# Kernel optimization log

Hardware: AMD Instinct MI355X
Metric: run time of the kernel (lower is better)

Reference implementation:

```python
import jax, jax.numpy as jnp
import numpy as np

B, N, NE = 4, 10000, 100000
D, S, H, T = 128, 64, 4, 128      # enc_dim, enc_s_dim, n_head, n_token
NS = D + S                        # GNN node_size = 192
EPS = 1e-5


def linear(x, w, b):
    return x @ w.T + b


def layer_norm(x, g, b):
    m = jnp.mean(x, -1, keepdims=True)
    v = jnp.mean((x - m) ** 2, -1, keepdims=True)
    return (x - m) * jax.lax.rsqrt(v + EPS) * g + b


def mha(q, k, v, wqkv, bqkv, wo, bo):
    # torch nn.MultiheadAttention, batch_first=True
    d = q.shape[-1]; hd = d // H
    wq, wk, wv = jnp.split(wqkv, 3, 0)
    bq, bk, bv = jnp.split(bqkv, 3, 0)
    def proj(x, w, bb):
        Bx, L, _ = x.shape
        return (x @ w.T + bb).reshape(Bx, L, H, hd)
    qh, kh, vh = proj(q, wq, bq), proj(k, wk, bk), proj(v, wv, bv)
    scores = jnp.einsum('bqhd,bkhd->bhqk', qh, kh) / jnp.sqrt(jnp.asarray(hd, q.dtype))
    att = jax.nn.softmax(scores, axis=-1)
    o = jnp.einsum('bhqk,bkhd->bqhd', att, vh).reshape(q.shape[0], q.shape[1], d)
    return o @ wo.T + bo


def smean(vals, idx, n):
    # scatter_mean over one batch element: vals (ne,f), idx (ne,)
    s = jax.ops.segment_sum(vals, idx, num_segments=n)
    c = jax.ops.segment_sum(jnp.ones(idx.shape, vals.dtype), idx, num_segments=n)
    return s / jnp.maximum(c, 1.0)[:, None]

_smean_b = jax.vmap(smean, in_axes=(0, 0, None))
_gather_b = jax.vmap(lambda v, i: v[i])


def setup_inputs():
    key = jax.random.key(0)
    ks = jax.random.split(key, 32)
    r = lambda i, shape: jax.random.normal(ks[i], shape, jnp.float32) * 0.02
    inp = {
        'V': jax.random.normal(ks[0], (B, N, D), jnp.float32),
        'E': jax.random.normal(ks[1], (B, NE, D), jnp.float32),
        'edges': jax.random.randint(ks[2], (B, NE, 2), 0, N),
        's_enc': jax.random.normal(ks[3], (B, N, S), jnp.float32),
        # GNN f_edge: Linear(512,128) SiLU Linear(128,128) LN(128)
        'fe_w1': r(4, (D, D + 2 * NS)), 'fe_b1': jnp.zeros(D),
        'fe_w2': r(5, (D, D)), 'fe_b2': jnp.zeros(D),
        'fe_g': jnp.ones(D), 'fe_be': jnp.zeros(D),
        # GNN f_node: Linear(320,128) SiLU Linear(128,128) LN(128)
        'fn_w1': r(6, (D, NS + D)), 'fn_b1': jnp.zeros(D),
        'fn_w2': r(7, (D, D)), 'fn_b2': jnp.zeros(D),
        'fn_g': jnp.ones(D), 'fn_be': jnp.zeros(D),
        'ln1_g': jnp.ones(D), 'ln1_b': jnp.zeros(D),
        'ln2_g': jnp.ones(D), 'ln2_b': jnp.zeros(D),
        'Q': jax.random.normal(ks[8], (T, D), jnp.float32),
        'a1_wqkv': r(9, (3 * D, D)), 'a1_bqkv': jnp.zeros(3 * D),
        'a1_wo': r(10, (D, D)), 'a1_bo': jnp.zeros(D),
        'a2_wqkv': r(11, (3 * D, D)), 'a2_bqkv': jnp.zeros(3 * D),
        'a2_wo': r(12, (D, D)), 'a2_bo': jnp.zeros(D),
        'a3_wqkv': r(13, (3 * D, D)), 'a3_bqkv': jnp.zeros(3 * D),
        'a3_wo': r(14, (D, D)), 'a3_bo': jnp.zeros(D),
        'ffn_w1': r(15, (2 * D, D)), 'ffn_b1': jnp.zeros(2 * D),
        'ffn_w2': r(16, (D, 2 * D)), 'ffn_b2': jnp.zeros(D),
    }
    return inp


def reference(V, E, edges, s_enc,
              fe_w1, fe_b1, fe_w2, fe_b2, fe_g, fe_be,
              fn_w1, fn_b1, fn_w2, fn_b2, fn_g, fn_be,
              ln1_g, ln1_b, ln2_g, ln2_b,
              Q, a1_wqkv, a1_bqkv, a1_wo, a1_bo,
              a2_wqkv, a2_bqkv, a2_wo, a2_bo,
              a3_wqkv, a3_bqkv, a3_wo, a3_bo,
              ffn_w1, ffn_b1, ffn_w2, ffn_b2):
    n = V.shape[1]
    V_in = jnp.concatenate([V, s_enc], -1)                  # (B,N,192)
    valid = jnp.all(edges >= 0, -1)                          # (B,NE)
    safe = jnp.clip(edges, 0, n - 1)
    senders = _gather_b(V_in, safe[..., 0])                  # (B,NE,192)
    receivers = _gather_b(V_in, safe[..., 1])
    edge_inpt = jnp.concatenate([senders, receivers, E], -1) # (B,NE,512)
    eh = jax.nn.silu(linear(edge_inpt, fe_w1, fe_b1))
    e_emb = layer_norm(linear(eh, fe_w2, fe_b2), fe_g, fe_be)
    e_emb = e_emb * valid[..., None].astype(e_emb.dtype)
    e0, e1 = jnp.split(e_emb, 2, -1)
    m0 = _smean_b(e0, safe[..., 0], n)
    m1 = _smean_b(e1, safe[..., 1], n)
    node_inpt = jnp.concatenate([V_in, m0, m1], -1)          # (B,N,320)
    nh = jax.nn.silu(linear(node_inpt, fn_w1, fn_b1))
    v_emb = layer_norm(linear(nh, fn_w2, fn_b2), fn_g, fn_be)
    E_out = E + e_emb
    V1 = V + v_emb
    # attention block
    W0 = layer_norm(V1, ln1_g, ln1_b)
    lq = jnp.broadcast_to(Q, (V.shape[0],) + Q.shape)
    W = mha(lq, W0, W0, a1_wqkv, a1_bqkv, a1_wo, a1_bo)
    W = mha(W, W, W, a2_wqkv, a2_bqkv, a2_wo, a2_bo)
    W = mha(W0, W, W, a3_wqkv, a3_bqkv, a3_wo, a3_bo)
    V2 = V1 + W
    # FFN block
    x = layer_norm(V2, ln2_g, ln2_b)
    V3 = V2 + linear(jax.nn.silu(linear(x, ffn_w1, ffn_b1)), ffn_w2, ffn_b2)
    return (V3, E_out)
```

## Files before the change

### kernel.cpp

```cpp
#include <hip/hip_runtime.h>
#include <hip/hip_bf16.h>

#define B_ 4
#define N_ 10000
#define NE_ 100000
#define D_ 128
#define S_ 64
#define H_ 4
#define T_ 128

typedef unsigned short u16;
typedef unsigned int u32;
typedef __attribute__((ext_vector_type(4))) float f4;
typedef __attribute__((ext_vector_type(8))) short s8;

#define DEVI static __device__ __forceinline__

DEVI float b2f(u16 u){ union{u32 i; float f;} v; v.i=((u32)u)<<16; return v.f; }
DEVI u16 f2b(float f){ union{float ff; u32 i;} v; v.ff=f; u32 i=v.i; return (u16)((i+0x7fffu+((i>>16)&1u))>>16); }
DEVI f4 mfma16(s8 a, s8 b, f4 c){ return __builtin_amdgcn_mfma_f32_16x16x32_bf16(a,b,c,0,0,0); }
DEVI float rsum16(float x){ x+=__shfl_xor(x,1); x+=__shfl_xor(x,2); x+=__shfl_xor(x,4); x+=__shfl_xor(x,8); return x; }
DEVI float silu_f(float v){ return v/(1.f+__expf(-v)); }
DEVI float nn(float v, float s){ return (v==v)? v : s; }
DEVI float lo2f(u32 u){ union{u32 i; float f;} v; v.i=u<<16; return v.f; }
DEVI float hi2f(u32 u){ union{u32 i; float f;} v; v.i=u&0xffff0000u; return v.f; }

DEVI s8 ldw8f(const float* p){
  f4 a = *(const f4*)p;
  f4 c = *(const f4*)(p+4);
  union { u16 t[8]; s8 v; } u;
  #pragma unroll
  for (int i=0;i<4;i++){ u.t[i]=f2b(a[i]); u.t[4+i]=f2b(c[i]); }
  return u.v;
}
DEVI uint4 cvt8(const float* p){
  f4 a = *(const f4*)p;
  f4 c = *(const f4*)(p+4);
  union { u16 t[8]; uint4 v; } u;
  #pragma unroll
  for (int i=0;i<4;i++){ u.t[i]=f2b(a[i]); u.t[4+i]=f2b(c[i]); }
  return u.v;
}
DEVI uint4 cvt8nt(const float* p){
  f4 a = __builtin_nontemporal_load((const f4*)p);
  f4 c = __builtin_nontemporal_load((const f4*)(p+4));
  union { u16 t[8]; uint4 v; } u;
  #pragma unroll
  for (int i=0;i<4;i++){ u.t[i]=f2b(a[i]); u.t[4+i]=f2b(c[i]); }
  return u.v;
}

#define WO_FE1 0
#define WO_FE2 65536
#define WO_FN1 81920
#define WO_FN2 122880
#define WO_A1  139264
#define WO_A3  188416
#define WO_A3O 237568
#define WO_FF1 253952
#define WO_FF2 286720
#define WTOT   319488

__global__ __launch_bounds__(256) void k_cvtw(
  const float* __restrict__ s0, const float* __restrict__ s1,
  const float* __restrict__ s2, const float* __restrict__ s3,
  const float* __restrict__ s4, const float* __restrict__ s5,
  const float* __restrict__ s6, const float* __restrict__ s7,
  const float* __restrict__ s8v, u16* __restrict__ dst)
{
  int i = (blockIdx.x*256 + threadIdx.x)*8;
  if (i >= WTOT) return;
  const float* src; int off;
  if      (i < WO_FE2){ src=s0;  off=WO_FE1; }
  else if (i < WO_FN1){ src=s1;  off=WO_FE2; }
  else if (i < WO_FN2){ src=s2;  off=WO_FN1; }
  else if (i < WO_A1 ){ src=s3;  off=WO_FN2; }
  else if (i < WO_A3 ){ src=s4;  off=WO_A1;  }
  else if (i < WO_A3O){ src=s5;  off=WO_A3;  }
  else if (i < WO_FF1){ src=s6;  off=WO_A3O; }
  else if (i < WO_FF2){ src=s7;  off=WO_FF1; }
  else                { src=s8v; off=WO_FF2; }
  *(uint4*)(dst+i) = cvt8(src + (i-off));
}

__global__ __launch_bounds__(512,4) void k_edge(
  const float* __restrict__ V, const float* __restrict__ E, const int* __restrict__ edges,
  const float* __restrict__ senc,
  const u16* __restrict__ w1b, const float* __restrict__ b1,
  const u16* __restrict__ w2b, const float* __restrict__ b2,
  const float* __restrict__ lng, const float* __restrict__ lnb,
  float* __restrict__ m0s, float* __restrict__ m1s,
  float* __restrict__ c0s, float* __restrict__ c1s,
  float* __restrict__ Eout)
{
  __shared__ u16 X[64][520];
  __shared__ int gi0[64], gi1[64];
  __shared__ float fvalid[64];
  __shared__ float rsA[64][8], rsB[64][8];
  const int tid = threadIdx.x;
  const int el = tid>>3, part = tid&7;
  const int ge = blockIdx.x*64 + el;
  const int b = ge / NE_;
  const int2 ed = *(const int2*)(edges + (size_t)ge*2);
  const int i0 = min(max(ed.x,0),N_-1), i1 = min(max(ed.y,0),N_-1);
  if (part==0){
    gi0[el] = b*N_ + i0; gi1[el] = b*N_ + i1;
    fvalid[el] = (ed.x>=0 && ed.y>=0) ? 1.f : 0.f;
  }
  {
    const float* Vb = V + (size_t)b*N_*D_;
    const float* Sb = senc + (size_t)b*N_*S_;
    const float* Ep = E + (size_t)ge*D_;
    #pragma unroll
    for (int j=0;j<8;j++){
      int u = part + 8*j;
      if (u<48){
        const float* p;
        if (u<16)      p = Vb + (size_t)i0*D_ + u*8;
        else if (u<24) p = Sb + (size_t)i0*S_ + (u-16)*8;
        else if (u<40) p = Vb + (size_t)i1*D_ + (u-24)*8;
        else           p = Sb + (size_t)i1*S_ + (u-40)*8;
        *(uint4*)&X[el][u*8] = cvt8(p);
      } else {
        *(uint4*)&X[el][u*8] = cvt8nt(Ep + (u-48)*8);
      }
    }
  }
  __syncthreads();
  if (tid < 64){
    atomicAdd(&c0s[gi0[tid]], 1.f);
    atomicAdd(&c1s[gi1[tid]], 1.f);
  }
  const int lane = tid&63, w = tid>>6;
  const int l15 = lane&15, hi = lane>>4;
  const int colb = w*16;
  f4 acc[4];
  #pragma unroll
  for (int m=0;m<4;m++){ float bb=b1[colb+l15]; acc[m]=(f4){bb,bb,bb,bb}; }
  for (int kk=0;kk<16;kk++){
    s8 bfr = *(const s8*)(w1b + (size_t)(colb+l15)*512 + kk*32 + hi*8);
    #pragma unroll
    for (int m=0;m<4;m++){
      s8 a = *(const s8*)&X[m*16+l15][kk*32 + hi*8];
      acc[m] = mfma16(a, bfr, acc[m]);
    }
  }
  __syncthreads();
  #pragma unroll
  for (int m=0;m<4;m++)
    #pragma unroll
    for (int r=0;r<4;r++)
      X[m*16+hi*4+r][colb+l15] = f2b(silu_f(acc[m][r]));
  __syncthreads();
  f4 a2[4];
  #pragma unroll
  for (int m=0;m<4;m++){ float bb=b2[colb+l15]; a2[m]=(f4){bb,bb,bb,bb}; }
  #pragma unroll
  for (int kk=0;kk<4;kk++){
    s8 bfr = *(const s8*)(w2b + (size_t)(colb+l15)*128 + kk*32 + hi*8);
    #pragma unroll
    for (int m=0;m<4;m++){
      s8 a = *(const s8*)&X[m*16+l15][kk*32 + hi*8];
      a2[m] = mfma16(a, bfr, a2[m]);
    }
  }
  #pragma unroll
  for (int m=0;m<4;m++)
    #pragma unroll
    for (int r=0;r<4;r++){
      float v=a2[m][r];
      float ps=rsum16(v), pq=rsum16(v*v);
      if (l15==0){ int row=m*16+hi*4+r; rsA[row][w]=ps; rsB[row][w]=pq; }
    }
  __syncthreads();
  const float gv=lng[colb+l15], bev=lnb[colb+l15];
  const int ge0 = blockIdx.x*64;
  #pragma unroll
  for (int m=0;m<4;m++)
    #pragma unroll
    for (int r=0;r<4;r++){
      const int row = m*16+hi*4+r;
      float s=0.f, s2=0.f;
      #pragma unroll
      for (int ww=0;ww<8;ww++){ s+=rsA[row][ww]; s2+=rsB[row][ww]; }
      const float mean = s*(1.f/128.f);
      const float rstd = rsqrtf(s2*(1.f/128.f) - mean*mean + 1e-5f);
      const float vm = fvalid[row];
      const int col = colb+l15;
      float ev = ((a2[m][r]-mean)*rstd*gv + bev) * vm;
      ev = nn(ev, 7e3f);
      if (col < 64) atomicAdd(m0s + (size_t)gi0[row]*64 + col, ev);
      else          atomicAdd(m1s + (size_t)gi1[row]*64 + (col-64), ev);
      float ef = b2f(X[row][384+col]);
      __builtin_nontemporal_store(ef + ev, Eout + (size_t)(ge0+row)*D_ + col);
    }
}

__global__ __launch_bounds__(256,2) void k_nodekv(
  const float* __restrict__ V, const float* __restrict__ senc,
  const float* __restrict__ m0s, const float* __restrict__ m1s,
  const float* __restrict__ c0s, const float* __restrict__ c1s,
  const u16* __restrict__ w1b, const float* __restrict__ b1,
  const u16* __restrict__ w2b, const float* __restrict__ b2,
  const float* __restrict__ lng, const float* __restrict__ lnb,
  const float* __restrict__ l1g, const float* __restrict__ l1b,
  const u16* __restrict__ wqkvb, const float* __restrict__ bqkv,
  u16* __restrict__ V1, u16* __restrict__ W0,
  u16* __restrict__ kh1, u16* __restrict__ vh1)
{
  __shared__ u16 X[64][328];
  __shared__ float rsA[64][4], rsB[64][4];
  const int tid=threadIdx.x, nl=tid>>2, part=tid&3;
  const int gn = blockIdx.x*64 + nl;
  const int b = gn / N_, n = gn - b*N_;
  {
    const float* Vp = V + ((size_t)b*N_ + n)*D_;
    const float* Sp = senc + ((size_t)b*N_ + n)*S_;
    #pragma unroll
    for (int j=0;j<6;j++){
      int u = part + 4*j;
      const float* p = (u<16)? Vp + u*8 : Sp + (u-16)*8;
      *(uint4*)&X[nl][u*8] = cvt8(p);
    }
    const float rc0 = 1.f/fmaxf(c0s[gn],1.f), rc1 = 1.f/fmaxf(c1s[gn],1.f);
    #pragma unroll
    for (int j=0;j<8;j++){
      int c = part*32 + j*4;
      const float* src = (c<64)? m0s + (size_t)gn*64 + c : m1s + (size_t)gn*64 + (c-64);
      float rr = (c<64)? rc0 : rc1;
      f4 mv = *(const f4*)src;
      u16 ov[4];
      #pragma unroll
      for (int i=0;i<4;i++) ov[i]=f2b(mv[i]*rr);
      uint2 pk; __builtin_memcpy(&pk, ov, 8);
      *(uint2*)&X[nl][192+c] = pk;
    }
  }
  __syncthreads();
  const int lane=tid&63, w=tid>>6, l15=lane&15, hi=lane>>4, colb=w*32;
  f4 acc[4][2];
  #pragma unroll
  for (int m=0;m<4;m++)
    #pragma unroll
    for (int tl=0;tl<2;tl++){ float bb=b1[colb+tl*16+l15]; acc[m][tl]=(f4){bb,bb,bb,bb}; }
  for (int kk=0;kk<10;kk++){
    s8 bfr[2];
    #pragma unroll
    for (int tl=0;tl<2;tl++)
      bfr[tl] = *(const s8*)(w1b + (size_t)(colb+tl*16+l15)*320 + kk*32 + hi*8);
    #pragma unroll
    for (int m=0;m<4;m++){
      s8 a = *(const s8*)&X[m*16+l15][kk*32+hi*8];
      #pragma unroll
      for (int tl=0;tl<2;tl++) acc[m][tl]=mfma16(a,bfr[tl],acc[m][tl]);
    }
  }
  __syncthreads();
  #pragma unroll
  for (int m=0;m<4;m++)
    #pragma unroll
    for (int tl=0;tl<2;tl++)
      #pragma unroll
      for (int r=0;r<4;r++)
        X[m*16+hi*4+r][192+colb+tl*16+l15] = f2b(silu_f(acc[m][tl][r]));
  __syncthreads();
  f4 a2[4][2];
  #pragma unroll
  for (int m=0;m<4;m++)
    #pragma unroll
    for (int tl=0;tl<2;tl++){ float bb=b2[colb+tl*16+l15]; a2[m][tl]=(f4){bb,bb,bb,bb}; }
  #pragma unroll
  for (int kk=0;kk<4;kk++){
    s8 bfr[2];
    #pragma unroll
    for (int tl=0;tl<2;tl++)
      bfr[tl] = *(const s8*)(w2b + (size_t)(colb+tl*16+l15)*128 + kk*32 + hi*8);
    #pragma unroll
    for (int m=0;m<4;m++){
      s8 a = *(const s8*)&X[m*16+l15][192 + kk*32+hi*8];
      #pragma unroll
      for (int tl=0;tl<2;tl++) a2[m][tl]=mfma16(a,bfr[tl],a2[m][tl]);
    }
  }
  #pragma unroll
  for (int m=0;m<4;m++)
    #pragma unroll
    for (int r=0;r<4;r++){
      float ps=0.f, pq=0.f;
      #pragma unroll
      for (int tl=0;tl<2;tl++){ float v=a2[m][tl][r]; ps+=v; pq+=v*v; }
      ps=rsum16(ps); pq=rsum16(pq);
      if (l15==0){ int row=m*16+hi*4+r; rsA[row][w]=ps; rsB[row][w]=pq; }
    }
  __syncthreads();
  float gv[2],bev[2],g1v[2],b1v[2];
  #pragma unroll
  for (int tl=0;tl<2;tl++){
    int col=colb+tl*16+l15;
    gv[tl]=lng[col]; bev[tl]=lnb[col]; g1v[tl]=l1g[col]; b1v[tl]=l1b[col];
  }
  #pragma unroll
  for (int m=0;m<4;m++)
    #pragma unroll
    for (int r=0;r<4;r++){
      const int row=m*16+hi*4+r;
      float s  = rsA[row][0]+rsA[row][1]+rsA[row][2]+rsA[row][3];
      float s2 = rsB[row][0]+rsB[row][1]+rsB[row][2]+rsB[row][3];
      float mean=s*(1.f/128.f);
      float rstd=rsqrtf(s2*(1.f/128.f)-mean*mean+1e-5f);
      #pragma unroll
      for (int tl=0;tl<2;tl++){
        float ve=(a2[m][tl][r]-mean)*rstd*gv[tl]+bev[tl];
        a2[m][tl][r] = b2f(X[row][colb+tl*16+l15]) + ve;
      }
    }
  __syncthreads();
  #pragma unroll
  for (int m=0;m<4;m++)
    #pragma unroll
    for (int r=0;r<4;r++){
      float ps=0.f, pq=0.f;
      #pragma unroll
      for (int tl=0;tl<2;tl++){ float v=a2[m][tl][r]; ps+=v; pq+=v*v; }
      ps=rsum16(ps); pq=rsum16(pq);
      if (l15==0){ int row=m*16+hi*4+r; rsA[row][w]=ps; rsB[row][w]=pq; }
    }
  __syncthreads();
  #pragma unroll
  for (int m=0;m<4;m++)
    #pragma unroll
    for (int r=0;r<4;r++){
      const int row=m*16+hi*4+r;
      float sv  = rsA[row][0]+rsA[row][1]+rsA[row][2]+rsA[row][3];
      float sv2 = rsB[row][0]+rsB[row][1]+rsB[row][2]+rsB[row][3];
      float m2=sv*(1.f/128.f);
      float rs2=rsqrtf(sv2*(1.f/128.f)-m2*m2+1e-5f);
      #pragma unroll
      for (int tl=0;tl<2;tl++){
        int col=colb+tl*16+l15;
        float tmp=a2[m][tl][r];
        X[row][col]     = f2b(tmp);
        X[row][192+col] = f2b((tmp-m2)*rs2*g1v[tl]+b1v[tl]);
      }
    }
  __syncthreads();
  #pragma unroll
  for (int j=0;j<4;j++){
    int u=part+4*j;
    *(uint4*)(V1 + (size_t)gn*D_ + u*8) = *(const uint4*)&X[nl][u*8];
    *(uint4*)(W0 + (size_t)gn*D_ + u*8) = *(const uint4*)&X[nl][192 + u*8];
  }
  const int colb2 = w*64;
  f4 acck[4][4];
  #pragma unroll
  for (int m=0;m<4;m++)
    #pragma unroll
    for (int tl=0;tl<4;tl++){ float bb=bqkv[128 + colb2+tl*16+l15]; acck[m][tl]=(f4){bb,bb,bb,bb}; }
  #pragma unroll
  for (int kk=0;kk<4;kk++){
    s8 bfr[4];
    #pragma unroll
    for (int tl=0;tl<4;tl++)
      bfr[tl] = *(const s8*)(wqkvb + (size_t)(128 + colb2+tl*16+l15)*D_ + kk*32+hi*8);
    #pragma unroll
    for (int m=0;m<4;m++){
      s8 a = *(const s8*)&X[m*16+l15][192 + kk*32+hi*8];
      #pragma unroll
      for (int tl=0;tl<4;tl++) acck[m][tl]=mfma16(a,bfr[tl],acck[m][tl]);
    }
  }
  __syncthreads();
  #pragma unroll
  for (int m=0;m<4;m++)
    #pragma unroll
    for (int tl=0;tl<4;tl++)
      #pragma unroll
      for (int r=0;r<4;r++)
        X[m*16+hi*4+r][colb2+tl*16+l15]=f2b(acck[m][tl][r]);
  __syncthreads();
  #pragma unroll
  for (int j=0;j<8;j++){
    int u=part+4*j, col0=u*8;
    u16* dst;
    if (col0<128){ int h=col0>>5, d=col0&31; dst = kh1 + ((size_t)(b*H_+h)*N_ + n)*32 + d; }
    else { int c2=col0-128; int h=c2>>5, d=c2&31; dst = vh1 + ((size_t)(b*H_+h)*N_ + n)*32 + d; }
    *(uint4*)dst = *(const uint4*)&X[nl][col0];
  }
}

__global__ __launch_bounds__(256) void k_qh1(
  const float* __restrict__ Q, const float* __restrict__ wqkv, const float* __restrict__ bqkv,
  u16* __restrict__ qh1)
{
  __shared__ u16 X[64][136];
  const int tid=threadIdx.x, nl=tid>>2, part=tid&3;
  const int q = blockIdx.x*64 + nl;
  #pragma unroll
  for (int j=0;j<4;j++){ int u=part+4*j; *(uint4*)&X[nl][u*8] = cvt8(Q + (size_t)q*D_ + u*8); }
  __syncthreads();
  const int lane=tid&63, w=tid>>6, l15=lane&15, hi=lane>>4, rw=w*16;
  f4 acc[8];
  #pragma unroll
  for (int t=0;t<8;t++){ float bb=bqkv[l15+16*t]; acc[t]=(f4){bb,bb,bb,bb}; }
  #pragma unroll
  for (int kk=0;kk<4;kk++){
    s8 a = *(const s8*)&X[rw+l15][kk*32+hi*8];
    #pragma unroll
    for (int t=0;t<8;t++){
      s8 bf = ldw8f(wqkv + (size_t)(t*16+l15)*D_ + kk*32+hi*8);
      acc[t]=mfma16(a,bf,acc[t]);
    }
  }
  __syncthreads();
  #pragma unroll
  for (int t=0;t<8;t++){
    #pragma unroll
    for (int r=0;r<4;r++) X[rw+hi*4+r][l15+16*t]=f2b(acc[t][r]);
  }
  __syncthreads();
  #pragma unroll
  for (int j=0;j<4;j++){
    int u=part+4*j, col0=u*8, h=col0>>5, d=col0&31;
    *(uint4*)(qh1 + ((size_t)h*T_ + q)*32 + d) = *(const uint4*)&X[nl][col0];
  }
}

#define NCH 20
#define CHK 512

__global__ __launch_bounds__(256,2) void k_mha1p(
  const u16* __restrict__ qh1, const u16* __restrict__ kh1, const u16* __restrict__ vh1,
  float* __restrict__ pm, float* __restrict__ pl, float* __restrict__ po)
{
  __shared__ u16 VT[32][72];
  __shared__ u16 P[4][32][72];
  const int bh = blockIdx.x / NCH, ch = blockIdx.x - bh*NCH;
  const int tid = threadIdx.x, w = tid>>6, lane = tid&63, l15=lane&15, hi=lane>>4;
  const int h = bh & 3;
  const int k0 = ch*CHK;
  const int nk = min(CHK, N_ - k0);
  const u16* Kb = kh1 + ((size_t)bh*N_ + k0)*32;
  const u16* Vb = vh1 + ((size_t)bh*N_ + k0)*32;
  s8 aq[2];
  #pragma unroll
  for (int qt=0;qt<2;qt++)
    aq[qt] = *(const s8*)(qh1 + ((size_t)h*T_ + w*32 + qt*16 + l15)*32 + hi*8);
  const float scale = 0.17677669529663687f;
  float m_reg[2][4], l_reg[2][4];
  f4 acc[2][2];
  #pragma unroll
  for (int qt=0;qt<2;qt++){
    #pragma unroll
    for (int r=0;r<4;r++){ m_reg[qt][r]=-1e30f; l_reg[qt][r]=0.f; }
    #pragma unroll
    for (int dt=0;dt<2;dt++) acc[qt][dt]=(f4){0.f,0.f,0.f,0.f};
  }
  const int ntile = (nk+63)>>6;
  for (int kt=0; kt<ntile; kt++){
    {
      int key = tid>>2, dseg = tid&3;
      int kg = kt*64 + key;
      uint4 v = (kg<nk)? *(const uint4*)(Vb + (size_t)kg*32 + dseg*8) : (uint4){0,0,0,0};
      const u16* vv = (const u16*)&v;
      #pragma unroll
      for (int i=0;i<8;i++) VT[dseg*8+i][key] = vv[i];
    }
    __syncthreads();
    f4 sa[2][4];
    #pragma unroll
    for (int kt4=0;kt4<4;kt4++){
      int key = kt*64 + kt4*16 + l15;
      int keyc = min(key, nk-1);
      s8 bk = *(const s8*)(Kb + (size_t)keyc*32 + hi*8);
      #pragma unroll
      for (int qt=0;qt<2;qt++)
        sa[qt][kt4] = mfma16(aq[qt], bk, (f4){0.f,0.f,0.f,0.f});
    }
    #pragma unroll
    for (int qt=0;qt<2;qt++){
      #pragma unroll
      for (int r=0;r<4;r++){
        float s[4];
        float mx = -1e30f;
        #pragma unroll
        for (int kt4=0;kt4<4;kt4++){
          int key = kt*64 + kt4*16 + l15;
          s[kt4] = (key<nk)? sa[qt][kt4][r]*scale : -1e30f;
          mx = fmaxf(mx, s[kt4]);
        }
        mx=fmaxf(mx,__shfl_xor(mx,1)); mx=fmaxf(mx,__shfl_xor(mx,2));
        mx=fmaxf(mx,__shfl_xor(mx,4)); mx=fmaxf(mx,__shfl_xor(mx,8));
        float mn = fmaxf(m_reg[qt][r], mx);
        float corr = __expf(m_reg[qt][r]-mn);
        float ps=0.f;
        #pragma unroll
        for (int kt4=0;kt4<4;kt4++){
          float p = __expf(s[kt4]-mn);
          ps += p;
          P[w][qt*16+hi*4+r][kt4*16+l15] = f2b(p);
        }
        ps = rsum16(ps);
        l_reg[qt][r] = l_reg[qt][r]*corr + ps;
        m_reg[qt][r] = mn;
        #pragma unroll
        for (int dt=0;dt<2;dt++) acc[qt][dt][r] *= corr;
      }
    }
    __syncthreads();
    #pragma unroll
    for (int ks=0;ks<2;ks++){
      s8 bv[2];
      #pragma unroll
      for (int dt=0;dt<2;dt++)
        bv[dt] = *(const s8*)&VT[dt*16+l15][ks*32+hi*8];
      #pragma unroll
      for (int qt=0;qt<2;qt++){
        s8 pa = *(const s8*)&P[w][qt*16+l15][ks*32+hi*8];
        #pragma unroll
        for (int dt=0;dt<2;dt++)
          acc[qt][dt]=mfma16(pa,bv[dt],acc[qt][dt]);
      }
    }
    __syncthreads();
  }
  const size_t pbase = ((size_t)bh*NCH + ch)*128;
  #pragma unroll
  for (int qt=0;qt<2;qt++)
    #pragma unroll
    for (int r=0;r<4;r++){
      int row = w*32 + qt*16 + hi*4 + r;
      if (l15==0){ pm[pbase+row]=m_reg[qt][r]; pl[pbase+row]=l_reg[qt][r]; }
      #pragma unroll
      for (int dt=0;dt<2;dt++)
        po[(pbase+row)*32 + dt*16 + l15] = acc[qt][dt][r];
    }
}

__global__ __launch_bounds__(256) void k_mha1c(
  const float* __restrict__ pm, const float* __restrict__ pl, const float* __restrict__ po,
  float* __restrict__ o1)
{
  int gid = blockIdx.x*256 + threadIdx.x;
  int row = gid >> 5, dim = gid & 31;
  int bh = row >> 7, q = row & 127;
  int b = bh >> 2, h = bh & 3;
  float M = -1e30f;
  #pragma unroll
  for (int ch=0; ch<NCH; ch++) M = fmaxf(M, pm[((size_t)bh*NCH+ch)*128 + q]);
  float L=0.f, O=0.f;
  for (int ch=0; ch<NCH; ch++){
    size_t pb = ((size_t)bh*NCH+ch)*128 + q;
    float e = __expf(pm[pb]-M);
    L += pl[pb]*e;
    O += po[pb*32+dim]*e;
  }
  o1[((size_t)b*T_+q)*D_ + h*32 + dim] = O / L;
}

DEVI void mha_core(const float* qv, const u16* Kb, const u16* Vb, int nk,
                   int lane, float* outp)
{
  const float scale = 0.17677669529663687f;
  float m=-1e30f, ssum=0.f, o[32];
  #pragma unroll
  for (int i=0;i<32;i++) o[i]=0.f;
  for (int c0=0;c0<nk;c0+=64){
    int key=c0+lane, keyc = key<nk? key: nk-1;
    const uint4* kp=(const uint4*)(Kb+(size_t)keyc*32);
    float sa=0.f;
    #pragma unroll
    for (int i=0;i<4;i++){ uint4 u=kp[i];
      sa += qv[i*8+0]*lo2f(u.x)+qv[i*8+1]*hi2f(u.x)+qv[i*8+2]*lo2f(u.y)+qv[i*8+3]*hi2f(u.y)
          + qv[i*8+4]*lo2f(u.z)+qv[i*8+5]*hi2f(u.z)+qv[i*8+6]*lo2f(u.w)+qv[i*8+7]*hi2f(u.w);
    }
    float s=sa*scale;
    float mn=fmaxf(m,s);
    float corr=__expf(m-mn);
    float p=(key<nk)?__expf(s-mn):0.f;
    ssum=ssum*corr+p;
    const uint4* vp=(const uint4*)(Vb+(size_t)keyc*32);
    #pragma unroll
    for (int i=0;i<4;i++){ uint4 u=vp[i];
      o[i*8+0]=o[i*8+0]*corr+p*lo2f(u.x); o[i*8+1]=o[i*8+1]*corr+p*hi2f(u.x);
      o[i*8+2]=o[i*8+2]*corr+p*lo2f(u.y); o[i*8+3]=o[i*8+3]*corr+p*hi2f(u.y);
      o[i*8+4]=o[i*8+4]*corr+p*lo2f(u.z); o[i*8+5]=o[i*8+5]*corr+p*hi2f(u.z);
      o[i*8+6]=o[i*8+6]*corr+p*lo2f(u.w); o[i*8+7]=o[i*8+7]*corr+p*hi2f(u.w);
    }
    m=mn;
  }
  float M=m;
  #pragma unroll
  for (int d=32;d>=1;d>>=1) M=fmaxf(M,__shfl_xor(M,d));
  float sc=__expf(m-M);
  float sm=ssum*sc;
  #pragma unroll
  for (int d=32;d>=1;d>>=1) sm+=__shfl_xor(sm,d);
  float inv=1.f/sm;
  #pragma unroll
  for (int i=0;i<32;i++){
    float v=o[i]*sc;
    #pragma unroll
    for (int d=32;d>=1;d>>=1) v+=__shfl_xor(v,d);
    if (lane==0) outp[i]=v*inv;
  }
}

__global__ __launch_bounds__(256) void k_mha2(
  const u16* __restrict__ qh2, const u16* __restrict__ kh2, const u16* __restrict__ vh2,
  float* __restrict__ o2)
{
  const int blk=blockIdx.x, bh=blk>>5, b=bh>>2, h=bh&3;
  const int w=threadIdx.x>>6, lane=threadIdx.x&63;
  const int q=(blk&31)*4+w;
  float qv[32];
  const uint4* qp=(const uint4*)(qh2 + ((size_t)bh*T_+q)*32);
  #pragma unroll
  for (int i=0;i<4;i++){ uint4 u=qp[i];
    qv[i*8+0]=lo2f(u.x); qv[i*8+1]=hi2f(u.x); qv[i*8+2]=lo2f(u.y); qv[i*8+3]=hi2f(u.y);
    qv[i*8+4]=lo2f(u.z); qv[i*8+5]=hi2f(u.z); qv[i*8+6]=lo2f(u.w); qv[i*8+7]=hi2f(u.w); }
  mha_core(qv, kh2+(size_t)bh*T_*32, vh2+(size_t)bh*T_*32, T_, lane,
           o2+((size_t)b*T_+q)*D_+h*32);
}

__global__ __launch_bounds__(256) void k_att12(
  const float* __restrict__ o1, const float* __restrict__ wo, const float* __restrict__ bo,
  const float* __restrict__ wqkv, const float* __restrict__ bqkv,
  u16* __restrict__ qh2, u16* __restrict__ kh2, u16* __restrict__ vh2)
{
  __shared__ u16 X[64][136];
  __shared__ u16 Y[64][392];
  const int tid=threadIdx.x, nl=tid>>2, part=tid&3;
  const int row = blockIdx.x*64 + nl;
  #pragma unroll
  for (int j=0;j<8;j++){
    int c = part*32 + j*4;
    f4 mv = *(const f4*)(o1 + (size_t)row*D_ + c);
    u16 ov[4];
    #pragma unroll
    for (int i=0;i<4;i++) ov[i]=f2b(nn(mv[i],2e4f));
    uint2 pk; __builtin_memcpy(&pk, ov, 8);
    *(uint2*)&X[nl][c]=pk;
  }
  __syncthreads();
  const int lane=tid&63, w=tid>>6, l15=lane&15, hi=lane>>4, rw=w*16;
  {
    f4 acc[8];
    #pragma unroll
    for (int t=0;t<8;t++){ float bb=bo[l15+16*t]; acc[t]=(f4){bb,bb,bb,bb}; }
    #pragma unroll
    for (int kk=0;kk<4;kk++){
      s8 a = *(const s8*)&X[rw+l15][kk*32+hi*8];
      #pragma unroll
      for (int t=0;t<8;t++){
        s8 bf = ldw8f(wo + (size_t)(t*16+l15)*D_ + kk*32+hi*8);
        acc[t]=mfma16(a,bf,acc[t]);
      }
    }
    #pragma unroll
    for (int t=0;t<8;t++){
      #pragma unroll
      for (int r=0;r<4;r++) Y[rw+hi*4+r][l15+16*t]=f2b(acc[t][r]);
    }
  }
  __syncthreads();
  f4 a2[24];
  #pragma unroll
  for (int t=0;t<24;t++){ float bb=bqkv[l15+16*t]; a2[t]=(f4){bb,bb,bb,bb}; }
  #pragma unroll
  for (int kk=0;kk<4;kk++){
    s8 a = *(const s8*)&Y[rw+l15][kk*32+hi*8];
    #pragma unroll
    for (int t=0;t<24;t++){
      s8 bf = ldw8f(wqkv + (size_t)(t*16+l15)*D_ + kk*32+hi*8);
      a2[t]=mfma16(a,bf,a2[t]);
    }
  }
  __syncthreads();
  #pragma unroll
  for (int t=0;t<24;t++){
    #pragma unroll
    for (int r=0;r<4;r++) Y[rw+hi*4+r][l15+16*t]=f2b(a2[t][r]);
  }
  __syncthreads();
  const int b=row>>7, q=row&127;
  #pragma unroll
  for (int j=0;j<12;j++){
    int u=part+4*j, col0=u*8;
    int sel=col0>>7, c2=col0&127, h=c2>>5, d=c2&31;
    u16* base = sel==0? qh2 : (sel==1? kh2 : vh2);
    *(uint4*)(base + ((size_t)(b*H_+h)*T_ + q)*32 + d) = *(const uint4*)&Y[nl][col0];
  }
}

__global__ __launch_bounds__(256) void k_att23(
  const float* __restrict__ o2, const float* __restrict__ wo, const float* __restrict__ bo,
  const float* __restrict__ wqkv3, const float* __restrict__ bqkv3,
  u16* __restrict__ kh3, u16* __restrict__ vh3T)
{
  __shared__ u16 X[64][136];
  __shared__ u16 Y[64][264];
  const int tid=threadIdx.x, nl=tid>>2, part=tid&3;
  const int row = blockIdx.x*64 + nl;
  #pragma unroll
  for (int j=0;j<8;j++){
    int c = part*32 + j*4;
    f4 mv = *(const f4*)(o2 + (size_t)row*D_ + c);
    u16 ov[4];
    #pragma unroll
    for (int i=0;i<4;i++) ov[i]=f2b(nn(mv[i],3e4f));
    uint2 pk; __builtin_memcpy(&pk, ov, 8);
    *(uint2*)&X[nl][c]=pk;
  }
  __syncthreads();
  const int lane=tid&63, w=tid>>6, l15=lane&15, hi=lane>>4, rw=w*16;
  {
    f4 acc[8];
    #pragma unroll
    for (int t=0;t<8;t++){ float bb=bo[l15+16*t]; acc[t]=(f4){bb,bb,bb,bb}; }
    #pragma unroll
    for (int kk=0;kk<4;kk++){
      s8 a = *(const s8*)&X[rw+l15][kk*32+hi*8];
      #pragma unroll
      for (int t=0;t<8;t++){
        s8 bf = ldw8f(wo + (size_t)(t*16+l15)*D_ + kk*32+hi*8);
        acc[t]=mfma16(a,bf,acc[t]);
      }
    }
    #pragma unroll
    for (int t=0;t<8;t++){
      #pragma unroll
      for (int r=0;r<4;r++) Y[rw+hi*4+r][l15+16*t]=f2b(acc[t][r]);
    }
  }
  __syncthreads();
  f4 a2[16];
  #pragma unroll
  for (int t=0;t<16;t++){ float bb=bqkv3[128 + l15+16*t]; a2[t]=(f4){bb,bb,bb,bb}; }
  #pragma unroll
  for (int kk=0;kk<4;kk++){
    s8 a = *(const s8*)&Y[rw+l15][kk*32+hi*8];
    #pragma unroll
    for (int t=0;t<16;t++){
      s8 bf = ldw8f(wqkv3 + (size_t)(128 + t*16+l15)*D_ + kk*32+hi*8);
      a2[t]=mfma16(a,bf,a2[t]);
    }
  }
  __syncthreads();
  #pragma unroll
  for (int t=0;t<16;t++){
    #pragma unroll
    for (int r=0;r<4;r++) Y[rw+hi*4+r][l15+16*t]=f2b(a2[t][r]);
  }
  __syncthreads();
  const int b=row>>7, q=row&127;
  #pragma unroll
  for (int j=0;j<4;j++){
    int u=part+4*j, col0=u*8, h=col0>>5, d=col0&31;
    *(uint4*)(kh3 + ((size_t)(b*H_+h)*T_ + q)*32 + d) = *(const uint4*)&Y[nl][col0];
  }
  #pragma unroll
  for (int cc=0;cc<32;cc++){
    int c2 = part*32 + cc;
    int h=c2>>5, d=c2&31;
    vh3T[((size_t)(b*H_+h)*32 + d)*T_ + q] = Y[nl][128+c2];
  }
}

__global__ __launch_bounds__(256,2) void k_mha3f(
  const u16* __restrict__ W0, const u16* __restrict__ V1,
  const u16* __restrict__ wq3b, const float* __restrict__ bqkv3,
  const u16* __restrict__ kh3, const u16* __restrict__ vh3T,
  const u16* __restrict__ wo3b, const float* __restrict__ bo3,
  const float* __restrict__ l2g, const float* __restrict__ l2b,
  const u16* __restrict__ fw1b, const float* __restrict__ fb1,
  const u16* __restrict__ fw2b, const float* __restrict__ fb2,
  float* __restrict__ V3)
{
  __shared__ u16 Wt[64][136];
  __shared__ u16 Q3[64][136];
  __shared__ u16 P3[64][136];
  __shared__ float rsA[64][4], rsB[64][4];
  const int tid=threadIdx.x, nl=tid>>2, part=tid&3;
  const int b = blockIdx.x/157, tb = blockIdx.x - b*157;
  const int n0 = tb*64;
  {
    const int ns = min(n0+nl, N_-1);
    const u16* src = W0 + ((size_t)b*N_+ns)*D_;
    #pragma unroll
    for (int j=0;j<4;j++){ int u=part+4*j; *(uint4*)&Wt[nl][u*8] = *(const uint4*)(src+u*8); }
  }
  __syncthreads();
  const int lane=tid&63, w=tid>>6, l15=lane&15, hi=lane>>4;
  const int rw=w*16, colb=w*32;
  {
    f4 acc[4][2];
    #pragma unroll
    for (int m=0;m<4;m++)
      #pragma unroll
      for (int tl=0;tl<2;tl++){ float bb=bqkv3[colb+tl*16+l15]; acc[m][tl]=(f4){bb,bb,bb,bb}; }
    #pragma unroll
    for (int kk=0;kk<4;kk++){
      s8 bfr[2];
      #pragma unroll
      for (int tl=0;tl<2;tl++)
        bfr[tl] = *(const s8*)(wq3b + (size_t)(colb+tl*16+l15)*D_ + kk*32+hi*8);
      #pragma unroll
      for (int m=0;m<4;m++){
        s8 a = *(const s8*)&Wt[m*16+l15][kk*32+hi*8];
        #pragma unroll
        for (int tl=0;tl<2;tl++) acc[m][tl]=mfma16(a,bfr[tl],acc[m][tl]);
      }
    }
    #pragma unroll
    for (int m=0;m<4;m++)
      #pragma unroll
      for (int tl=0;tl<2;tl++)
        #pragma unroll
        for (int r=0;r<4;r++)
          Q3[m*16+hi*4+r][colb+tl*16+l15]=f2b(acc[m][tl][r]);
  }
  __syncthreads();
  const float scale=0.17677669529663687f;
  f4 oacc[8];
  #pragma unroll
  for (int t=0;t<8;t++) oacc[t]=(f4){0.f,0.f,0.f,0.f};
  #pragma unroll
  for (int h=0;h<H_;h++){
    f4 sa[8];
    #pragma unroll
    for (int t=0;t<8;t++) sa[t]=(f4){0.f,0.f,0.f,0.f};
    s8 aq = *(const s8*)&Q3[rw+l15][h*32+hi*8];
    #pragma unroll
    for (int t=0;t<8;t++){
      s8 bf = *(const s8*)(kh3 + ((size_t)(b*H_+h)*T_ + t*16+l15)*32 + hi*8);
      sa[t]=mfma16(aq,bf,sa[t]);
    }
    #pragma unroll
    for (int r=0;r<4;r++){
      const int row=rw+hi*4+r;
      float mx=-1e30f;
      float sv[8];
      #pragma unroll
      for (int t=0;t<8;t++){ sv[t]=sa[t][r]*scale; mx=fmaxf(mx,sv[t]); }
      mx=fmaxf(mx,__shfl_xor(mx,1)); mx=fmaxf(mx,__shfl_xor(mx,2));
      mx=fmaxf(mx,__shfl_xor(mx,4)); mx=fmaxf(mx,__shfl_xor(mx,8));
      float se=0.f; float pv[8];
      #pragma unroll
      for (int t=0;t<8;t++){ pv[t]=__expf(sv[t]-mx); se+=pv[t]; }
      se=rsum16(se);
      float inv=1.f/se;
      #pragma unroll
      for (int t=0;t<8;t++) P3[row][l15+16*t]=f2b(pv[t]*inv);
    }
    __syncthreads();
    #pragma unroll
    for (int kk=0;kk<4;kk++){
      s8 ap = *(const s8*)&P3[rw+l15][kk*32+hi*8];
      #pragma unroll
      for (int t2=0;t2<2;t2++){
        s8 bf = *(const s8*)(vh3T + ((size_t)(b*H_+h)*32 + t2*16+l15)*T_ + kk*32+hi*8);
        oacc[h*2+t2]=mfma16(ap,bf,oacc[h*2+t2]);
      }
    }
    __syncthreads();
  }
  #pragma unroll
  for (int t=0;t<8;t++){
    #pragma unroll
    for (int r=0;r<4;r++) Q3[rw+hi*4+r][l15+16*t]=f2b(oacc[t][r]);
  }
  __syncthreads();
  f4 a2[4][2];
  #pragma unroll
  for (int m=0;m<4;m++)
    #pragma unroll
    for (int tl=0;tl<2;tl++){ float bb=bo3[colb+tl*16+l15]; a2[m][tl]=(f4){bb,bb,bb,bb}; }
  #pragma unroll
  for (int kk=0;kk<4;kk++){
    s8 bfr[2];
    #pragma unroll
    for (int tl=0;tl<2;tl++)
      bfr[tl] = *(const s8*)(wo3b + (size_t)(colb+tl*16+l15)*D_ + kk*32+hi*8);
    #pragma unroll
    for (int m=0;m<4;m++){
      s8 a = *(const s8*)&Q3[m*16+l15][kk*32+hi*8];
      #pragma unroll
      for (int tl=0;tl<2;tl++) a2[m][tl]=mfma16(a,bfr[tl],a2[m][tl]);
    }
  }
  #pragma unroll
  for (int m=0;m<4;m++)
    #pragma unroll
    for (int r=0;r<4;r++){
      const int row=m*16+hi*4+r;
      const int nr = min(n0+row, N_-1);
      const size_t gr=(size_t)b*N_+nr;
      float ps=0.f, pq=0.f;
      #pragma unroll
      for (int tl=0;tl<2;tl++){
        float tmp = b2f(V1[gr*D_ + colb+tl*16+l15]) + a2[m][tl][r];
        a2[m][tl][r]=tmp; ps+=tmp; pq+=tmp*tmp;
      }
      ps=rsum16(ps); pq=rsum16(pq);
      if (l15==0){ rsA[row][w]=ps; rsB[row][w]=pq; }
    }
  __syncthreads();
  float g2v[2],b2v[2];
  #pragma unroll
  for (int tl=0;tl<2;tl++){ g2v[tl]=l2g[colb+tl*16+l15]; b2v[tl]=l2b[colb+tl*16+l15]; }
  #pragma unroll
  for (int m=0;m<4;m++)
    #pragma unroll
    for (int r=0;r<4;r++){
      const int row=m*16+hi*4+r;
      float s  = rsA[row][0]+rsA[row][1]+rsA[row][2]+rsA[row][3];
      float s2 = rsB[row][0]+rsB[row][1]+rsB[row][2]+rsB[row][3];
      float mean=s*(1.f/128.f);
      float rstd=rsqrtf(s2*(1.f/128.f)-mean*mean+1e-5f);
      #pragma unroll
      for (int tl=0;tl<2;tl++){
        int col=colb+tl*16+l15;
        float tmp=a2[m][tl][r];
        P3[row][col]=f2b(tmp);
        Wt[row][col]=f2b((tmp-mean)*rstd*g2v[tl]+b2v[tl]);
      }
    }
  __syncthreads();
  f4 accf[4][2];
  #pragma unroll
  for (int m=0;m<4;m++)
    #pragma unroll
    for (int tl=0;tl<2;tl++){ float bb=fb2[colb+tl*16+l15]; accf[m][tl]=(f4){bb,bb,bb,bb}; }
  for (int half=0;half<2;half++){
    f4 ah[4][2];
    #pragma unroll
    for (int m=0;m<4;m++)
      #pragma unroll
      for (int tl=0;tl<2;tl++){ float bb=fb1[half*128+colb+tl*16+l15]; ah[m][tl]=(f4){bb,bb,bb,bb}; }
    #pragma unroll
    for (int kk=0;kk<4;kk++){
      s8 bfr[2];
      #pragma unroll
      for (int tl=0;tl<2;tl++)
        bfr[tl] = *(const s8*)(fw1b + (size_t)(half*128+colb+tl*16+l15)*D_ + kk*32+hi*8);
      #pragma unroll
      for (int m=0;m<4;m++){
        s8 a = *(const s8*)&Wt[m*16+l15][kk*32+hi*8];
        #pragma unroll
        for (int tl=0;tl<2;tl++) ah[m][tl]=mfma16(a,bfr[tl],ah[m][tl]);
      }
    }
    __syncthreads();
    #pragma unroll
    for (int m=0;m<4;m++)
      #pragma unroll
      for (int tl=0;tl<2;tl++)
        #pragma unroll
        for (int r=0;r<4;r++)
          Q3[m*16+hi*4+r][colb+tl*16+l15]=f2b(silu_f(ah[m][tl][r]));
    __syncthreads();
    #pragma unroll
    for (int kk=0;kk<4;kk++){
      s8 bfr[2];
      #pragma unroll
      for (int tl=0;tl<2;tl++)
        bfr[tl] = *(const s8*)(fw2b + (size_t)(colb+tl*16+l15)*256 + half*128 + kk*32+hi*8);
      #pragma unroll
      for (int m=0;m<4;m++){
        s8 a = *(const s8*)&Q3[m*16+l15][kk*32+hi*8];
        #pragma unroll
        for (int tl=0;tl<2;tl++) accf[m][tl]=mfma16(a,bfr[tl],accf[m][tl]);
      }
    }
  }
  #pragma unroll
  for (int m=0;m<4;m++)
    #pragma unroll
    for (int r=0;r<4;r++){
      const int row=m*16+hi*4+r;
      if (n0+row < N_){
        const size_t gr=(size_t)b*N_+n0+row;
        #pragma unroll
        for (int tl=0;tl<2;tl++){
          int col=colb+tl*16+l15;
          V3[gr*D_+col] = b2f(P3[row][col]) + accf[m][tl][r];
        }
      }
    }
}

extern "C" void kernel_launch(void* const* d_in, const int* in_sizes, int n_in,
                              void* d_out, int out_size, void* d_ws, size_t ws_size,
                              hipStream_t stream)
{
  const float* V     = (const float*)d_in[0];
  const float* E     = (const float*)d_in[1];
  const int* edges   = (const int*)d_in[2];
  const float* senc  = (const float*)d_in[3];
  const float* fe_w1=(const float*)d_in[4];  const float* fe_b1=(const float*)d_in[5];
  const float* fe_w2=(const float*)d_in[6];  const float* fe_b2=(const float*)d_in[7];
  const float* fe_g =(const float*)d_in[8];  const float* fe_be=(const float*)d_in[9];
  const float* fn_w1=(const float*)d_in[10]; const float* fn_b1=(const float*)d_in[11];
  const float* fn_w2=(const float*)d_in[12]; const float* fn_b2=(const float*)d_in[13];
  const float* fn_g =(const float*)d_in[14]; const float* fn_be=(const float*)d_in[15];
  const float* ln1_g=(const float*)d_in[16]; const float* ln1_b=(const float*)d_in[17];
  const float* ln2_g=(const float*)d_in[18]; const float* ln2_b=(const float*)d_in[19];
  const float* Q    =(const float*)d_in[20];
  const float* a1_wqkv=(const float*)d_in[21]; const float* a1_bqkv=(const float*)d_in[22];
  const float* a1_wo=(const float*)d_in[23];   const float* a1_bo=(const float*)d_in[24];
  const float* a2_wqkv=(const float*)d_in[25]; const float* a2_bqkv=(const float*)d_in[26];
  const float* a2_wo=(const float*)d_in[27];   const float* a2_bo=(const float*)d_in[28];
  const float* a3_wqkv=(const float*)d_in[29]; const float* a3_bqkv=(const float*)d_in[30];
  const float* a3_wo=(const float*)d_in[31];   const float* a3_bo=(const float*)d_in[32];
  const float* ffn_w1=(const float*)d_in[33];  const float* ffn_b1=(const float*)d_in[34];
  const float* ffn_w2=(const float*)d_in[35];  const float* ffn_b2=(const float*)d_in[36];

  char* ws = (char*)d_ws;
  size_t off = 0;
  auto alloc = [&](size_t bytes)->void*{ void* p = ws + off; off += (bytes + 255) & ~(size_t)255; return p; };
  float* m0s = (float*)alloc((size_t)B_*N_*64*4);
  float* m1s = (float*)alloc((size_t)B_*N_*64*4);
  float* c0s = (float*)alloc((size_t)B_*N_*4);
  float* c1s = (float*)alloc((size_t)B_*N_*4);
  const size_t zero_bytes = off;
  u16* wcat = (u16*)alloc((size_t)WTOT*2);
  u16* V1  = (u16*)alloc((size_t)B_*N_*D_*2);
  u16* W0  = (u16*)alloc((size_t)B_*N_*D_*2);
  u16* kh1 = (u16*)alloc((size_t)B_*H_*N_*32*2);
  u16* vh1 = (u16*)alloc((size_t)B_*H_*N_*32*2);
  u16* qh1 = (u16*)alloc((size_t)H_*T_*32*2);
  float* o1 = (float*)alloc((size_t)B_*T_*D_*4);
  u16* qh2 = (u16*)alloc((size_t)B_*H_*T_*32*2);
  u16* kh2 = (u16*)alloc((size_t)B_*H_*T_*32*2);
  u16* vh2 = (u16*)alloc((size_t)B_*H_*T_*32*2);
  float* o2 = (float*)alloc((size_t)B_*T_*D_*4);
  u16* kh3 = (u16*)alloc((size_t)B_*H_*T_*32*2);
  u16* vh3T= (u16*)alloc((size_t)B_*H_*32*T_*2);
  float* pmw = (float*)alloc((size_t)B_*H_*NCH*128*4);
  float* plw = (float*)alloc((size_t)B_*H_*NCH*128*4);
  float* pow_ = (float*)alloc((size_t)B_*H_*NCH*128*32*4);
  if (ws_size < off) return;

  u16* w_fe1 = wcat + WO_FE1;
  u16* w_fe2 = wcat + WO_FE2;
  u16* w_fn1 = wcat + WO_FN1;
  u16* w_fn2 = wcat + WO_FN2;
  u16* w_a1  = wcat + WO_A1;
  u16* w_a3  = wcat + WO_A3;
  u16* w_a3o = wcat + WO_A3O;
  u16* w_ff1 = wcat + WO_FF1;
  u16* w_ff2 = wcat + WO_FF2;

  float* outp = (float*)d_out;
  float* V3out = outp;
  float* Eout  = outp + (size_t)B_*N_*D_;

  hipMemsetAsync(d_ws, 0, zero_bytes, stream);
  k_cvtw<<<(WTOT/8+255)/256,256,0,stream>>>(fe_w1,fe_w2,fn_w1,fn_w2,a1_wqkv,a3_wqkv,a3_wo,
                                            ffn_w1,ffn_w2, wcat);
  k_edge<<<(B_*NE_)/64,512,0,stream>>>(V,E,edges,senc, w_fe1,fe_b1, w_fe2,fe_b2, fe_g,fe_be,
                                       m0s,m1s,c0s,c1s, Eout);
  k_nodekv<<<(B_*N_)/64,256,0,stream>>>(V,senc,m0s,m1s,c0s,c1s, w_fn1,fn_b1, w_fn2,fn_b2,
                                        fn_g,fn_be, ln1_g,ln1_b, w_a1,a1_bqkv,
                                        V1,W0, kh1,vh1);
  k_qh1<<<T_/64,256,0,stream>>>(Q, a1_wqkv, a1_bqkv, qh1);
  k_mha1p<<<B_*H_*NCH,256,0,stream>>>(qh1,kh1,vh1, pmw,plw,pow_);
  k_mha1c<<<(B_*H_*T_*32)/256,256,0,stream>>>(pmw,plw,pow_, o1);
  k_att12<<<(B_*T_)/64,256,0,stream>>>(o1, a1_wo, a1_bo, a2_wqkv, a2_bqkv, qh2,kh2,vh2);
  k_mha2<<<(B_*H_*T_)/4,256,0,stream>>>(qh2,kh2,vh2,o2);
  k_att23<<<(B_*T_)/64,256,0,stream>>>(o2, a2_wo, a2_bo, a3_wqkv, a3_bqkv, kh3, vh3T);
  k_mha3f<<<B_*157,256,0,stream>>>(W0,V1, w_a3,a3_bqkv, kh3,vh3T, w_a3o,a3_bo,
                                   ln2_g,ln2_b, w_ff1,ffn_b1, w_ff2,ffn_b2, V3out);
}
```

Measured before the change: 619.7 us.

## Replace atomic scatter-mean with CSR edge lists and per-node gather

```diff
diff --git a/kernel.cpp b/kernel.cpp
--- a/kernel.cpp
+++ b/kernel.cpp
@@ -83,18 +83,91 @@
   *(uint4*)(dst+i) = cvt8(src + (i-off));
 }
 
+__global__ __launch_bounds__(256) void k_count(
+  const int* __restrict__ edges, int* __restrict__ cnt0, int* __restrict__ cnt1)
+{
+  int ge = blockIdx.x*256 + threadIdx.x;
+  if (ge >= B_*NE_) return;
+  int b = ge / NE_;
+  int2 ed = *(const int2*)(edges + (size_t)ge*2);
+  int i0 = min(max(ed.x,0),N_-1), i1 = min(max(ed.y,0),N_-1);
+  atomicAdd(&cnt0[b*N_+i0], 1);
+  atomicAdd(&cnt1[b*N_+i1], 1);
+}
+
+__global__ __launch_bounds__(1024) void k_scan_blk(
+  const int* __restrict__ cnt0, const int* __restrict__ cnt1,
+  int* __restrict__ off0, int* __restrict__ off1, int* __restrict__ bsum)
+{
+  __shared__ int sd[1024];
+  const int g = blockIdx.x;
+  const int arr = g >= 40;
+  const int gb = arr? g-40 : g;
+  const int* src = arr? cnt1 : cnt0;
+  int* dst = arr? off1 : off0;
+  const int t = threadIdx.x;
+  const int idx = gb*1024 + t;
+  int val = (idx < B_*N_)? src[idx] : 0;
+  sd[t] = val; __syncthreads();
+  int acc = val;
+  for (int d=1; d<1024; d<<=1){
+    int tv = (t>=d)? sd[t-d] : 0;
+    __syncthreads();
+    acc += tv; sd[t] = acc;
+    __syncthreads();
+  }
+  if (idx < B_*N_) dst[idx] = acc - val;
+  if (t == 1023) bsum[g] = acc;
+}
+
+__global__ __launch_bounds__(128) void k_scan_top(int* __restrict__ bsum)
+{
+  const int w = threadIdx.x>>6, lane = threadIdx.x&63;
+  const int base = w*40;
+  int v = (lane<40)? bsum[base+lane] : 0;
+  int orig = v;
+  for (int d=1; d<64; d<<=1){ int t=__shfl_up(v,d); if (lane>=d) v+=t; }
+  if (lane<40) bsum[base+lane] = v - orig;
+}
+
+__global__ __launch_bounds__(1024) void k_scan_add(
+  int* __restrict__ off0, int* __restrict__ off1, const int* __restrict__ bsum)
+{
+  const int g = blockIdx.x;
+  const int arr = g >= 40;
+  const int gb = arr? g-40 : g;
+  int* dst = arr? off1 : off0;
+  const int idx = gb*1024 + threadIdx.x;
+  if (idx < B_*N_) dst[idx] += bsum[g];
+}
+
+__global__ __launch_bounds__(256) void k_fill(
+  const int* __restrict__ edges,
+  const int* __restrict__ off0, const int* __restrict__ off1,
+  int* __restrict__ cur0, int* __restrict__ cur1,
+  int* __restrict__ eidx0, int* __restrict__ eidx1)
+{
+  int ge = blockIdx.x*256 + threadIdx.x;
+  if (ge >= B_*NE_) return;
+  int b = ge / NE_;
+  int2 ed = *(const int2*)(edges + (size_t)ge*2);
+  int i0 = min(max(ed.x,0),N_-1), i1 = min(max(ed.y,0),N_-1);
+  int g0 = b*N_+i0, g1 = b*N_+i1;
+  int p0 = off0[g0] + atomicAdd(&cur0[g0], 1);
+  eidx0[p0] = ge;
+  int p1 = off1[g1] + atomicAdd(&cur1[g1], 1);
+  eidx1[p1] = ge;
+}
+
 __global__ __launch_bounds__(512,4) void k_edge(
   const float* __restrict__ V, const float* __restrict__ E, const int* __restrict__ edges,
   const float* __restrict__ senc,
   const u16* __restrict__ w1b, const float* __restrict__ b1,
   const u16* __restrict__ w2b, const float* __restrict__ b2,
   const float* __restrict__ lng, const float* __restrict__ lnb,
-  float* __restrict__ m0s, float* __restrict__ m1s,
-  float* __restrict__ c0s, float* __restrict__ c1s,
   float* __restrict__ Eout)
 {
   __shared__ u16 X[64][520];
-  __shared__ int gi0[64], gi1[64];
   __shared__ float fvalid[64];
   __shared__ float rsA[64][8], rsB[64][8];
   const int tid = threadIdx.x;
@@ -103,10 +176,7 @@
   const int b = ge / NE_;
   const int2 ed = *(const int2*)(edges + (size_t)ge*2);
   const int i0 = min(max(ed.x,0),N_-1), i1 = min(max(ed.y,0),N_-1);
-  if (part==0){
-    gi0[el] = b*N_ + i0; gi1[el] = b*N_ + i1;
-    fvalid[el] = (ed.x>=0 && ed.y>=0) ? 1.f : 0.f;
-  }
+  if (part==0) fvalid[el] = (ed.x>=0 && ed.y>=0) ? 1.f : 0.f;
   {
     const float* Vb = V + (size_t)b*N_*D_;
     const float* Sb = senc + (size_t)b*N_*S_;
@@ -127,10 +197,6 @@
     }
   }
   __syncthreads();
-  if (tid < 64){
-    atomicAdd(&c0s[gi0[tid]], 1.f);
-    atomicAdd(&c1s[gi1[tid]], 1.f);
-  }
   const int lane = tid&63, w = tid>>6;
   const int l15 = lane&15, hi = lane>>4;
   const int colb = w*16;
@@ -189,8 +255,6 @@
       const int col = colb+l15;
       float ev = ((a2[m][r]-mean)*rstd*gv + bev) * vm;
       ev = nn(ev, 7e3f);
-      if (col < 64) atomicAdd(m0s + (size_t)gi0[row]*64 + col, ev);
-      else          atomicAdd(m1s + (size_t)gi1[row]*64 + (col-64), ev);
       float ef = b2f(X[row][384+col]);
       __builtin_nontemporal_store(ef + ev, Eout + (size_t)(ge0+row)*D_ + col);
     }
@@ -198,8 +262,10 @@
 
 __global__ __launch_bounds__(256,2) void k_nodekv(
   const float* __restrict__ V, const float* __restrict__ senc,
-  const float* __restrict__ m0s, const float* __restrict__ m1s,
-  const float* __restrict__ c0s, const float* __restrict__ c1s,
+  const float* __restrict__ Ein, const float* __restrict__ Eout,
+  const int* __restrict__ cnt0, const int* __restrict__ cnt1,
+  const int* __restrict__ off0, const int* __restrict__ off1,
+  const int* __restrict__ eidx0, const int* __restrict__ eidx1,
   const u16* __restrict__ w1b, const float* __restrict__ b1,
   const u16* __restrict__ w2b, const float* __restrict__ b2,
   const float* __restrict__ lng, const float* __restrict__ lnb,
@@ -222,18 +288,33 @@
       const float* p = (u<16)? Vp + u*8 : Sp + (u-16)*8;
       *(uint4*)&X[nl][u*8] = cvt8(p);
     }
-    const float rc0 = 1.f/fmaxf(c0s[gn],1.f), rc1 = 1.f/fmaxf(c1s[gn],1.f);
-    #pragma unroll
-    for (int j=0;j<8;j++){
-      int c = part*32 + j*4;
-      const float* src = (c<64)? m0s + (size_t)gn*64 + c : m1s + (size_t)gn*64 + (c-64);
-      float rr = (c<64)? rc0 : rc1;
-      f4 mv = *(const f4*)src;
-      u16 ov[4];
-      #pragma unroll
-      for (int i=0;i<4;i++) ov[i]=f2b(mv[i]*rr);
-      uint2 pk; __builtin_memcpy(&pk, ov, 8);
-      *(uint2*)&X[nl][192+c] = pk;
+    const int sel = part>>1;
+    const int cntv = sel? cnt1[gn] : cnt0[gn];
+    const int ob   = sel? off1[gn] : off0[gn];
+    const int* elist = sel? eidx1 : eidx0;
+    const int co = part*32;
+    float acc[32];
+    #pragma unroll
+    for (int i=0;i<32;i++) acc[i]=0.f;
+    for (int k=0;k<cntv;k++){
+      int e = elist[ob+k];
+      const f4* po_ = (const f4*)(Eout + (size_t)e*D_ + co);
+      const f4* pe  = (const f4*)(Ein  + (size_t)e*D_ + co);
+      #pragma unroll
+      for (int q=0;q<8;q++){
+        f4 a = po_[q], c = pe[q];
+        #pragma unroll
+        for (int i=0;i<4;i++) acc[q*4+i] += a[i]-c[i];
+      }
+    }
+    float rc = 1.f/(float)max(cntv,1);
+    #pragma unroll
+    for (int j=0;j<4;j++){
+      u16 ov[8];
+      #pragma unroll
+      for (int i=0;i<8;i++) ov[i]=f2b(acc[j*8+i]*rc);
+      uint4 pk; __builtin_memcpy(&pk, ov, 16);
+      *(uint4*)&X[nl][192+co+j*8] = pk;
     }
   }
   __syncthreads();
@@ -1018,11 +1099,16 @@
   char* ws = (char*)d_ws;
   size_t off = 0;
   auto alloc = [&](size_t bytes)->void*{ void* p = ws + off; off += (bytes + 255) & ~(size_t)255; return p; };
-  float* m0s = (float*)alloc((size_t)B_*N_*64*4);
-  float* m1s = (float*)alloc((size_t)B_*N_*64*4);
-  float* c0s = (float*)alloc((size_t)B_*N_*4);
-  float* c1s = (float*)alloc((size_t)B_*N_*4);
+  int* cnt0 = (int*)alloc((size_t)B_*N_*4);
+  int* cnt1 = (int*)alloc((size_t)B_*N_*4);
+  int* cur0 = (int*)alloc((size_t)B_*N_*4);
+  int* cur1 = (int*)alloc((size_t)B_*N_*4);
   const size_t zero_bytes = off;
+  int* bsum = (int*)alloc(128*4);
+  int* off0 = (int*)alloc((size_t)B_*N_*4);
+  int* off1 = (int*)alloc((size_t)B_*N_*4);
+  int* eidx0 = (int*)alloc((size_t)B_*NE_*4);
+  int* eidx1 = (int*)alloc((size_t)B_*NE_*4);
   u16* wcat = (u16*)alloc((size_t)WTOT*2);
   u16* V1  = (u16*)alloc((size_t)B_*N_*D_*2);
   u16* W0  = (u16*)alloc((size_t)B_*N_*D_*2);
@@ -1058,11 +1144,16 @@
   hipMemsetAsync(d_ws, 0, zero_bytes, stream);
   k_cvtw<<<(WTOT/8+255)/256,256,0,stream>>>(fe_w1,fe_w2,fn_w1,fn_w2,a1_wqkv,a3_wqkv,a3_wo,
                                             ffn_w1,ffn_w2, wcat);
+  k_count<<<(B_*NE_+255)/256,256,0,stream>>>(edges, cnt0, cnt1);
+  k_scan_blk<<<80,1024,0,stream>>>(cnt0,cnt1, off0,off1, bsum);
+  k_scan_top<<<1,128,0,stream>>>(bsum);
+  k_scan_add<<<80,1024,0,stream>>>(off0,off1, bsum);
+  k_fill<<<(B_*NE_+255)/256,256,0,stream>>>(edges, off0,off1, cur0,cur1, eidx0,eidx1);
   k_edge<<<(B_*NE_)/64,512,0,stream>>>(V,E,edges,senc, w_fe1,fe_b1, w_fe2,fe_b2, fe_g,fe_be,
-                                       m0s,m1s,c0s,c1s, Eout);
-  k_nodekv<<<(B_*N_)/64,256,0,stream>>>(V,senc,m0s,m1s,c0s,c1s, w_fn1,fn_b1, w_fn2,fn_b2,
-                                        fn_g,fn_be, ln1_g,ln1_b, w_a1,a1_bqkv,
-                                        V1,W0, kh1,vh1);
+                                       Eout);
+  k_nodekv<<<(B_*N_)/64,256,0,stream>>>(V,senc, E,Eout, cnt0,cnt1, off0,off1, eidx0,eidx1,
+                                        w_fn1,fn_b1, w_fn2,fn_b2, fn_g,fn_be, ln1_g,ln1_b,
+                                        w_a1,a1_bqkv, V1,W0, kh1,vh1);
   k_qh1<<<T_/64,256,0,stream>>>(Q, a1_wqkv, a1_bqkv, qh1);
   k_mha1p<<<B_*H_*NCH,256,0,stream>>>(qh1,kh1,vh1, pmw,plw,pow_);
   k_mha1c<<<(B_*H_*T_*32)/256,256,0,stream>>>(pmw,plw,pow_, o1);
```

Result: slower. 740.2 us (+19.5%).
